# Performance work log

Measured on AMD Instinct MI355X. Metric: run time of the kernel, lower is better.

## Reference

```python
import jax, jax.numpy as jnp
import numpy as np

DISP = 8 // 2  # self.disp = disp // 2


def setup_inputs() -> dict:
    key = jax.random.key(0)
    inputs = jax.random.normal(key, (1, 16, 9, 256, 256), dtype=jnp.float32)
    return {"inputs": inputs}


def reference(inputs) -> jnp.ndarray:
    # inputs: [b, c, A, h, w]
    b, c, A, h, w = inputs.shape
    ds = jnp.arange(-DISP, DISP + 1)            # [D] disparity hypotheses
    a_off = jnp.arange(A) - A // 2              # [A] angular offsets
    t = ds[:, None] * a_off[None, :]            # [D, A] shift per (d, a)

    # roll by t with zero-fill == gather from index (i - t), masked to in-range
    hi = jnp.arange(h)[None, None, :] - t[:, :, None]   # [D, A, h]
    wi = jnp.arange(w)[None, None, :] - t[:, :, None]   # [D, A, w]
    h_valid = (hi >= 0) & (hi < h)
    w_valid = (wi >= 0) & (wi < w)
    hi = jnp.clip(hi, 0, h - 1)
    wi = jnp.clip(wi, 0, w - 1)

    # broadcast index arrays to [D, A, h, w]
    a_idx = jnp.arange(A)[None, :, None, None]
    h_idx = hi[:, :, :, None]
    w_idx = wi[:, :, None, :]
    gathered = inputs[:, :, a_idx, h_idx, w_idx]        # [b, c, D, A, h, w]

    mask = (h_valid[:, :, :, None] & w_valid[:, :, None, :])  # [D, A, h, w]
    out = gathered * mask.astype(inputs.dtype)

    # torch.stack(..., dim=1) -> [b, D, c, A, h, w]
    return jnp.transpose(out, (0, 2, 1, 3, 4, 5))
```

## Files before the change

kernel.cpp:

```cpp
#include <hip/hip_runtime.h>


#define RTILE 16

typedef float vf4 __attribute__((ext_vector_type(4)));

template<int TR>
__device__ __forceinline__ void emit_plane(const float* __restrict__ lds_t,
                                           float* __restrict__ oplane,
                                           int g0, int t, int tq,
                                           int tx, int ty)
{
    for (int yb = ty; yb < RTILE; yb += 4) {
        int y = g0 + yb + t;
        if (y < 0 || y >= 256) continue;
        const float* __restrict__ lrow = lds_t + yb * 256;
        float* __restrict__ orow = oplane + (long)y * 256;

        int m2 = tx - tq;
        int m2c = m2 < 0 ? 0 : (m2 > 63 ? 63 : m2);
        vf4 B = *reinterpret_cast<const vf4*>(lrow + 4 * m2c);
        float w0, w1, w2, w3;
        if (TR == 0) {
            w0 = B.x; w1 = B.y; w2 = B.z; w3 = B.w;
        } else {
            int m1 = m2 - 1;
            int m1c = m1 < 0 ? 0 : (m1 > 63 ? 63 : m1);
            vf4 A = *reinterpret_cast<const vf4*>(lrow + 4 * m1c);
            float cc[8] = {A.x, A.y, A.z, A.w, B.x, B.y, B.z, B.w};
            w0 = cc[4 - TR]; w1 = cc[5 - TR];
            w2 = cc[6 - TR]; w3 = cc[7 - TR];
        }
        int x0 = 4 * tx;
        int lo = t, hi = 256 + t;
        vf4 v;
        v.x = (x0 + 0 >= lo && x0 + 0 < hi) ? w0 : 0.f;
        v.y = (x0 + 1 >= lo && x0 + 1 < hi) ? w1 : 0.f;
        v.z = (x0 + 2 >= lo && x0 + 2 < hi) ? w2 : 0.f;
        v.w = (x0 + 3 >= lo && x0 + 3 < hi) ? w3 : 0.f;
        *reinterpret_cast<vf4*>(orow + x0) = v;
    }
}

__global__ __launch_bounds__(256) void cost_volume_kernel(
    const float* __restrict__ in, float* __restrict__ out)
{
    __shared__ float lds_t[RTILE * 256];

    int ca = blockIdx.y;
    int c = ca / 9;
    int a = ca - c * 9;
    int a4 = a - 4;
    int g0 = blockIdx.x * RTILE;

    int tx = threadIdx.x;
    int ty = threadIdx.y;

    const float* __restrict__ slice = in + (long)ca * 65536;
    #pragma unroll
    for (int r0 = 0; r0 < RTILE; r0 += 4) {
        int r = r0 + ty;
        *reinterpret_cast<vf4*>(&lds_t[r * 256 + tx * 4]) =
            *reinterpret_cast<const vf4*>(slice + (long)(g0 + r) * 256 + tx * 4);
    }
    __syncthreads();

    #pragma unroll
    for (int d = 0; d < 9; ++d) {
        int t = (d - 4) * a4;
        float* __restrict__ oplane = out + ((long)(d * 16 + c) * 9 + a) * 65536L;
        int tq = t >> 2;
        switch (t & 3) {
        case 0: emit_plane<0>(lds_t, oplane, g0, t, tq, tx, ty); break;
        case 1: emit_plane<1>(lds_t, oplane, g0, t, tq, tx, ty); break;
        case 2: emit_plane<2>(lds_t, oplane, g0, t, tq, tx, ty); break;
        case 3: emit_plane<3>(lds_t, oplane, g0, t, tq, tx, ty); break;
        }

        int zn = t < 0 ? -t : t;
        int z0 = t > 0 ? 0 : 256 + t;
        if (zn && ty == (d & 3) && (int)blockIdx.x < zn) {
            float* __restrict__ orow = oplane + (long)(z0 + (int)blockIdx.x) * 256;
            vf4 z = {0.f, 0.f, 0.f, 0.f};
            *reinterpret_cast<vf4*>(orow + tx * 4) = z;
        }
    }
}

extern "C" void kernel_launch(void* const* d_in, const int* in_sizes, int n_in,
                              void* d_out, int out_size, void* d_ws, size_t ws_size,
                              hipStream_t stream)
{
    const float* in = (const float*)d_in[0];
    float* out = (float*)d_out;

    dim3 block(64, 4, 1);
    dim3 grid(16, 144, 1);
    cost_volume_kernel<<<grid, block, 0, stream>>>(in, out);
}
```

Before: 76.74 us.

## Assign one block per output plane, read input directly, use nontemporal stores

Drops the LDS tile shared across the nine disparities and launches one block per (c,a,d) output plane. Each block streams the whole plane, reading the shifted input rows from global memory (cached in L2) and writing with nontemporal stores. Zero rows are now written inline instead of by a separate pass, and the edge masks become bitwise ANDs. In exchange, each input slice is read nine times from cache rather than once per tile, and the grid shrinks to 1296 blocks that each run longer.

```diff
diff --git a/kernel.cpp b/kernel.cpp
--- a/kernel.cpp
+++ b/kernel.cpp
@@ -1,89 +1,69 @@
 #include <hip/hip_runtime.h>
 
 
-#define RTILE 16
-
 typedef float vf4 __attribute__((ext_vector_type(4)));
+typedef unsigned int uint;
 
 template<int TR>
-__device__ __forceinline__ void emit_plane(const float* __restrict__ lds_t,
+__device__ __forceinline__ void plane_loop(const float* __restrict__ slice,
                                            float* __restrict__ oplane,
-                                           int g0, int t, int tq,
-                                           int tx, int ty)
+                                           int t, int tx, int ty)
 {
-    for (int yb = ty; yb < RTILE; yb += 4) {
-        int y = g0 + yb + t;
-        if (y < 0 || y >= 256) continue;
-        const float* __restrict__ lrow = lds_t + yb * 256;
-        float* __restrict__ orow = oplane + (long)y * 256;
+    int tq = t >> 2;
+    int m2 = tx - tq;
+    int m2c = m2 < 0 ? 0 : (m2 > 63 ? 63 : m2);
+    int m1 = m2 - 1;
+    int m1c = m1 < 0 ? 0 : (m1 > 63 ? 63 : m1);
+    int x0 = 4 * tx;
+    uint k0 = (x0 + 0 >= t && x0 + 0 < 256 + t) ? 0xFFFFFFFFu : 0u;
+    uint k1 = (x0 + 1 >= t && x0 + 1 < 256 + t) ? 0xFFFFFFFFu : 0u;
+    uint k2 = (x0 + 2 >= t && x0 + 2 < 256 + t) ? 0xFFFFFFFFu : 0u;
+    uint k3 = (x0 + 3 >= t && x0 + 3 < 256 + t) ? 0xFFFFFFFFu : 0u;
 
-        int m2 = tx - tq;
-        int m2c = m2 < 0 ? 0 : (m2 > 63 ? 63 : m2);
-        vf4 B = *reinterpret_cast<const vf4*>(lrow + 4 * m2c);
-        float w0, w1, w2, w3;
-        if (TR == 0) {
-            w0 = B.x; w1 = B.y; w2 = B.z; w3 = B.w;
-        } else {
-            int m1 = m2 - 1;
-            int m1c = m1 < 0 ? 0 : (m1 > 63 ? 63 : m1);
-            vf4 A = *reinterpret_cast<const vf4*>(lrow + 4 * m1c);
-            float cc[8] = {A.x, A.y, A.z, A.w, B.x, B.y, B.z, B.w};
-            w0 = cc[4 - TR]; w1 = cc[5 - TR];
-            w2 = cc[6 - TR]; w3 = cc[7 - TR];
+    for (int y = ty; y < 256; y += 4) {
+        int yy = y - t;
+        vf4 v = {0.f, 0.f, 0.f, 0.f};
+        if (yy >= 0 && yy < 256) {
+            const float* __restrict__ row = slice + yy * 256;
+            vf4 B = *reinterpret_cast<const vf4*>(row + 4 * m2c);
+            float w0, w1, w2, w3;
+            if (TR == 0) {
+                w0 = B.x; w1 = B.y; w2 = B.z; w3 = B.w;
+            } else {
+                vf4 A = *reinterpret_cast<const vf4*>(row + 4 * m1c);
+                float cc[8] = {A.x, A.y, A.z, A.w, B.x, B.y, B.z, B.w};
+                w0 = cc[4 - TR]; w1 = cc[5 - TR];
+                w2 = cc[6 - TR]; w3 = cc[7 - TR];
+            }
+            v.x = __uint_as_float(__float_as_uint(w0) & k0);
+            v.y = __uint_as_float(__float_as_uint(w1) & k1);
+            v.z = __uint_as_float(__float_as_uint(w2) & k2);
+            v.w = __uint_as_float(__float_as_uint(w3) & k3);
         }
-        int x0 = 4 * tx;
-        int lo = t, hi = 256 + t;
-        vf4 v;
-        v.x = (x0 + 0 >= lo && x0 + 0 < hi) ? w0 : 0.f;
-        v.y = (x0 + 1 >= lo && x0 + 1 < hi) ? w1 : 0.f;
-        v.z = (x0 + 2 >= lo && x0 + 2 < hi) ? w2 : 0.f;
-        v.w = (x0 + 3 >= lo && x0 + 3 < hi) ? w3 : 0.f;
-        *reinterpret_cast<vf4*>(orow + x0) = v;
+        __builtin_nontemporal_store(v, reinterpret_cast<vf4*>(oplane + y * 256 + x0));
     }
 }
 
 __global__ __launch_bounds__(256) void cost_volume_kernel(
     const float* __restrict__ in, float* __restrict__ out)
 {
-    __shared__ float lds_t[RTILE * 256];
-
-    int ca = blockIdx.y;
+    int ca = blockIdx.x;
+    int d  = blockIdx.y;
     int c = ca / 9;
     int a = ca - c * 9;
-    int a4 = a - 4;
-    int g0 = blockIdx.x * RTILE;
+    int t = (d - 4) * (a - 4);
+
+    const float* __restrict__ slice = in + (long)ca * 65536;
+    float* __restrict__ oplane = out + ((long)(d * 16 + c) * 9 + a) * 65536L;
 
     int tx = threadIdx.x;
     int ty = threadIdx.y;
 
-    const float* __restrict__ slice = in + (long)ca * 65536;
-    #pragma unroll
-    for (int r0 = 0; r0 < RTILE; r0 += 4) {
-        int r = r0 + ty;
-        *reinterpret_cast<vf4*>(&lds_t[r * 256 + tx * 4]) =
-            *reinterpret_cast<const vf4*>(slice + (long)(g0 + r) * 256 + tx * 4);
-    }
-    __syncthreads();
-
-    #pragma unroll
-    for (int d = 0; d < 9; ++d) {
-        int t = (d - 4) * a4;
-        float* __restrict__ oplane = out + ((long)(d * 16 + c) * 9 + a) * 65536L;
-        int tq = t >> 2;
-        switch (t & 3) {
-        case 0: emit_plane<0>(lds_t, oplane, g0, t, tq, tx, ty); break;
-        case 1: emit_plane<1>(lds_t, oplane, g0, t, tq, tx, ty); break;
-        case 2: emit_plane<2>(lds_t, oplane, g0, t, tq, tx, ty); break;
-        case 3: emit_plane<3>(lds_t, oplane, g0, t, tq, tx, ty); break;
-        }
-
-        int zn = t < 0 ? -t : t;
-        int z0 = t > 0 ? 0 : 256 + t;
-        if (zn && ty == (d & 3) && (int)blockIdx.x < zn) {
-            float* __restrict__ orow = oplane + (long)(z0 + (int)blockIdx.x) * 256;
-            vf4 z = {0.f, 0.f, 0.f, 0.f};
-            *reinterpret_cast<vf4*>(orow + tx * 4) = z;
-        }
+    switch (t & 3) {
+    case 0: plane_loop<0>(slice, oplane, t, tx, ty); break;
+    case 1: plane_loop<1>(slice, oplane, t, tx, ty); break;
+    case 2: plane_loop<2>(slice, oplane, t, tx, ty); break;
+    case 3: plane_loop<3>(slice, oplane, t, tx, ty); break;
     }
 }
 
@@ -95,6 +75,6 @@
     float* out = (float*)d_out;
 
     dim3 block(64, 4, 1);
-    dim3 grid(16, 144, 1);
+    dim3 grid(144, 9, 1);
     cost_volume_kernel<<<grid, block, 0, stream>>>(in, out);
 }
```

Result: faster. 74.17 us (-3.4%).
